# Optimization experiments

Measured on AMD Instinct MI355X. Metric: run time of the kernel, lower is better.

The kernel has to match this reference:

```python
import jax, jax.numpy as jnp
import numpy as np

KERNEL_MUL = 2.0
KERNEL_NUM = 5


def setup_inputs() -> dict:
    key = jax.random.key(0)
    k1, k2 = jax.random.split(key)
    B, Ns, Nt, K = 4, 2048, 2048, 32
    source = jax.random.normal(k1, (B, Ns, K), dtype=jnp.float32)
    target = jax.random.normal(k2, (B, Nt, K), dtype=jnp.float32)
    return {"source": source, "target": target}


def _mmd_rbf(source, target):
    # source: [B, Ns, K], target: [B, Nt, K]
    Ns = source.shape[1]
    Nt = target.shape[1]
    n_samples = Ns + Nt
    total = jnp.concatenate([source, target], axis=1)  # [B, N, K]
    # Pairwise squared L2 via Gram trick (avoids [B, N, N, K] broadcast tensor)
    sq = jnp.sum(total * total, axis=-1)  # [B, N]
    gram = jnp.einsum('bik,bjk->bij', total, total)  # [B, N, N]
    L2 = sq[:, :, None] + sq[:, None, :] - 2.0 * gram  # [B, N, N]
    # Multi-bandwidth RBF kernel sum
    bw = jnp.sum(L2, axis=(1, 2), keepdims=True) / (n_samples ** 2 - n_samples + 1e-8)  # [B,1,1]
    bw = bw / (KERNEL_MUL ** (KERNEL_NUM // 2))
    # Small fixed loop over bandwidths; accumulate to avoid [K_num, B, N, N] stack.
    kernel = jnp.zeros_like(L2)
    for i in range(KERNEL_NUM):
        kernel = kernel + jnp.exp(-L2 / (bw * (KERNEL_MUL ** i)) + 1e-8)
    # Quadrant means
    N = Ns
    XX = kernel[:, :N, :N].mean(axis=(1, 2))
    YY = kernel[:, N:, N:].mean(axis=(1, 2))
    XY = kernel[:, :N, N:].mean(axis=(1, 2))
    YX = kernel[:, N:, :N].mean(axis=(1, 2))
    return XX + YY - XY - YX  # [B]


def reference(source, target):
    return _mmd_rbf(source, target)
```

## Files before the change

### kernel.cpp

```cpp
#include <hip/hip_runtime.h>
#include <hip/hip_bf16.h>


#define NPTS 4096
#define HALF 2048
#define KDIM 32
#define T3   128
#define NTB3 32
#define NPAIR3 528
#define GRIDX 176
#define SPREAD 64

#define WS_SQ    0
#define WS_PART  65536
#define WS_QUAD  133120
#define WS_FRAG  147456
#define WS_NEED  (147456 + 4 * NPTS * 128)

typedef __attribute__((ext_vector_type(8))) short short8v;
typedef __attribute__((ext_vector_type(4))) float f32x4;

__device__ __forceinline__ float fast_exp2(float x) {
#if __has_builtin(__builtin_amdgcn_exp2f)
  return __builtin_amdgcn_exp2f(x);
#else
  return exp2f(x);
#endif
}

__device__ __forceinline__ unsigned int bf16_rne(float x) {
  unsigned int u = __float_as_uint(x);
  return (u + 0x7fffu + ((u >> 16) & 1u)) >> 16;
}

__device__ __forceinline__ const float* point_ptr(const float* __restrict__ src,
                                                  const float* __restrict__ tgt,
                                                  int b, int p) {
  return (p < HALF) ? src + ((size_t)b * HALF + p) * KDIM
                    : tgt + ((size_t)b * HALF + (p - HALF)) * KDIM;
}

__global__ void __launch_bounds__(64)
mmd_pass1(const float* __restrict__ src, const float* __restrict__ tgt,
          float* __restrict__ sqArr, double* __restrict__ part1,
          double* __restrict__ quadbuf,
          unsigned char* __restrict__ frags, int preFlag) {
  const int b = blockIdx.y;
  const int tid = threadIdx.x;
  const int p = blockIdx.x * 64 + tid;

  if (blockIdx.x == 0) {
#pragma unroll
    for (int i = 0; i < 4; ++i)
      quadbuf[b * 4 * SPREAD + i * 64 + tid] = 0.0;
  }

  const float* __restrict__ xp = point_ptr(src, tgt, b, p);
  float x[KDIM];
#pragma unroll
  for (int q = 0; q < 8; ++q) {
    float4 v = reinterpret_cast<const float4*>(xp)[q];
    x[4*q+0] = v.x; x[4*q+1] = v.y; x[4*q+2] = v.z; x[4*q+3] = v.w;
  }
  float s0 = 0.f, s1 = 0.f, s2 = 0.f, s3 = 0.f;
#pragma unroll
  for (int q = 0; q < 8; ++q) {
    s0 = fmaf(x[4*q+0], x[4*q+0], s0);
    s1 = fmaf(x[4*q+1], x[4*q+1], s1);
    s2 = fmaf(x[4*q+2], x[4*q+2], s2);
    s3 = fmaf(x[4*q+3], x[4*q+3], s3);
  }
  const float sq = (s0 + s1) + (s2 + s3);
  sqArr[(size_t)b * NPTS + p] = sq;

  if (preFlag) {
    unsigned int hw[16], lw[16];
#pragma unroll
    for (int e = 0; e < 16; ++e) {
      const float xa = x[2*e], xb = x[2*e+1];
      const unsigned int ha = bf16_rne(xa);
      const unsigned int la = bf16_rne(xa - __uint_as_float(ha << 16));
      const unsigned int hb = bf16_rne(xb);
      const unsigned int lb = bf16_rne(xb - __uint_as_float(hb << 16));
      hw[e] = ha | (hb << 16);
      lw[e] = la | (lb << 16);
    }
    uint4* dst = reinterpret_cast<uint4*>(frags + (size_t)(b * NPTS + p) * 128);
#pragma unroll
    for (int c = 0; c < 4; ++c)
      dst[c] = make_uint4(hw[4*c], hw[4*c+1], hw[4*c+2], hw[4*c+3]);
#pragma unroll
    for (int c = 0; c < 4; ++c)
      dst[4 + c] = make_uint4(lw[4*c], lw[4*c+1], lw[4*c+2], lw[4*c+3]);
  }

  __shared__ float lx[64][KDIM + 1];
#pragma unroll
  for (int k = 0; k < KDIM; ++k) lx[tid][k] = x[k];
  __syncthreads();

  double* slot = part1 + ((size_t)b * 64 + blockIdx.x) * 33;
  if (tid < 32) {
    float ps = 0.f;
#pragma unroll 16
    for (int r = 0; r < 64; ++r) ps += lx[r][tid];
    slot[1 + tid] = (double)ps;
  }
  float w = sq;
#pragma unroll
  for (int off = 32; off > 0; off >>= 1) w += __shfl_down(w, off, 64);
  if (tid == 0) slot[0] = (double)w;
}

__device__ __forceinline__ short8v lds_frag(const unsigned char* base, int p,
                                            int half, int lk) {
  const int slot = (half * 4 + lk) ^ (p & 7);
  return *reinterpret_cast<const short8v*>(base + p * 128 + slot * 16);
}

template <bool PRE>
__global__ void __launch_bounds__(512, 6)
mmd_pass3(const float* __restrict__ src, const float* __restrict__ tgt,
          const float* __restrict__ sqArr, const double* __restrict__ part1,
          const unsigned char* __restrict__ frags,
          double* __restrict__ quadbuf) {
  const int bid = blockIdx.x;
  const int b = blockIdx.y;
  const int tid = threadIdx.x;
  const int lane = tid & 63;
  const int w = tid >> 6;
  const int lm = lane & 15;
  const int lk = lane >> 4;
  const int wr = w & 3;
  const int wc = w >> 2;

  __shared__ __align__(16) unsigned char fragA[T3 * 128];
  __shared__ __align__(16) unsigned char fragB[T3 * 128];
  __shared__ float s_sqA[T3], s_sqB[T3];
  __shared__ double red[33];
  __shared__ float s_nc4;
  __shared__ double wsum[8];

  const float* __restrict__ sqG = sqArr + (size_t)b * NPTS;
  const uint4* __restrict__ gfr =
      reinterpret_cast<const uint4*>(frags) + (size_t)b * NPTS * 8;

  if (tid < 33) {
    double s = 0.0;
#pragma unroll 16
    for (int blk = 0; blk < 64; ++blk)
      s += part1[((size_t)b * 64 + blk) * 33 + tid];
    red[tid] = s;
  }
  __syncthreads();
  if (tid == 0) {
    double ssq = red[0], s2 = 0.0;
    for (int k = 1; k <= 32; ++k) s2 += red[k] * red[k];
    const double N = (double)NPTS;
    double bw = (2.0 * N * ssq - 2.0 * s2) / (N * N - N + 1e-8);
    bw *= 0.25;
    s_nc4 = (float)(-1.4426950408889634 / (bw * 16.0));
  }

  int bxA[3], byA[3];
#pragma unroll
  for (int it = 0; it < 3; ++it) {
    const int pi = bid + it * GRIDX;
    int y = (int)((sqrtf((float)(8 * pi + 1)) - 1.0f) * 0.5f);
    while ((y + 1) * (y + 2) / 2 <= pi) ++y;
    while (y * (y + 1) / 2 > pi) --y;
    byA[it] = y; bxA[it] = pi - y * (y + 1) / 2;
  }

  {
    const int bx = bxA[0], by = byA[0];
    if constexpr (PRE) {
#pragma unroll
      for (int i = 0; i < 2; ++i) {
        const int g = tid + i * 512;
        const int p = g >> 3, s = g & 7;
        const int d = p * 8 + (s ^ (p & 7));
        reinterpret_cast<uint4*>(fragA)[d] = gfr[(size_t)bx * 1024 + g];
        reinterpret_cast<uint4*>(fragB)[d] = gfr[(size_t)by * 1024 + g];
      }
    } else if (tid < 256) {
      const int pt = tid & 127;
      const bool isB = tid >= 128;
      const float* fp = point_ptr(src, tgt, b, (isB ? by : bx) * T3 + pt);
      unsigned int hw[16], lw[16];
#pragma unroll
      for (int e = 0; e < 16; ++e) {
        const float xa = fp[2*e], xb = fp[2*e+1];
        const unsigned int ha = bf16_rne(xa);
        const unsigned int la = bf16_rne(xa - __uint_as_float(ha << 16));
        const unsigned int hb = bf16_rne(xb);
        const unsigned int lb = bf16_rne(xb - __uint_as_float(hb << 16));
        hw[e] = ha | (hb << 16);
        lw[e] = la | (lb << 16);
      }
      uint4* dst = reinterpret_cast<uint4*>((isB ? fragB : fragA) + pt * 128);
#pragma unroll
      for (int s = 0; s < 8; ++s) {
        const unsigned int* s4 = (s < 4) ? &hw[s * 4] : &lw[(s - 4) * 4];
        dst[s ^ (pt & 7)] = make_uint4(s4[0], s4[1], s4[2], s4[3]);
      }
    }
    if (tid < 128) s_sqA[tid] = sqG[bx * T3 + tid];
    else if (tid < 256) s_sqB[tid - 128] = sqG[by * T3 + (tid - 128)];
  }
  __syncthreads();

  const float nc4 = s_nc4;
  const float m2nc = -2.0f * nc4;

  for (int it = 0; it < 3; ++it) {
    const int bx = bxA[it], by = byA[it];

    double accd = 0.0;
#pragma unroll
    for (int cg = 0; cg < 4; ++cg) {
      const int pb = wc * 64 + cg * 16 + lm;
      const short8v Bh = lds_frag(fragB, pb, 0, lk);
      const short8v Bl = lds_frag(fragB, pb, 1, lk);
      const float sjn = s_sqB[pb] * nc4;
#pragma unroll
      for (int rg = 0; rg < 2; ++rg) {
        const int pa = wr * 32 + rg * 16 + lm;
        const short8v Ah = lds_frag(fragA, pa, 0, lk);
        const short8v Al = lds_frag(fragA, pa, 1, lk);
        const float4 sqi4 = *reinterpret_cast<const float4*>(
            &s_sqA[wr * 32 + rg * 16 + lk * 4]);
        const float sin_[4] = {sqi4.x * nc4, sqi4.y * nc4,
                               sqi4.z * nc4, sqi4.w * nc4};
        f32x4 accP = {0.f, 0.f, 0.f, 0.f};
        f32x4 accQ = {0.f, 0.f, 0.f, 0.f};
        accP = __builtin_amdgcn_mfma_f32_16x16x32_bf16(Ah, Bh, accP, 0, 0, 0);
        accQ = __builtin_amdgcn_mfma_f32_16x16x32_bf16(Ah, Bl, accQ, 0, 0, 0);
        accP = __builtin_amdgcn_mfma_f32_16x16x32_bf16(Al, Bl, accP, 0, 0, 0);
        accQ = __builtin_amdgcn_mfma_f32_16x16x32_bf16(Al, Bh, accQ, 0, 0, 0);
        float rs = 0.f;
#pragma unroll
        for (int reg = 0; reg < 4; ++reg) {
          const float dot = accP[reg] + accQ[reg];
          const float arg = fmaf(dot, m2nc, sin_[reg] + sjn);
          float e = fast_exp2(arg);
          float s = e;
          e *= e; s += e;
          e *= e; s += e;
          e *= e; s += e;
          e *= e; s += e;
          rs += s;
        }
        accd += (double)rs;
      }
    }

#pragma unroll
    for (int off = 32; off > 0; off >>= 1) accd += __shfl_down(accd, off, 64);
    if (lane == 0) wsum[w] = accd;

    __syncthreads();

    if (tid == 0) {
      double tot = 0.0;
#pragma unroll
      for (int ww = 0; ww < 8; ++ww) tot += wsum[ww];
      const int rh = (bx >= NTB3 / 2) ? 1 : 0;
      const int ch = (by >= NTB3 / 2) ? 1 : 0;
      const int q  = (rh << 1) | ch;
      const int qT = (ch << 1) | rh;
      const int slot = (bx + by * NTB3) & (SPREAD - 1);
      atomicAdd(&quadbuf[(((b << 2) | q) * SPREAD) + slot], tot);
      if (bx != by)
        atomicAdd(&quadbuf[(((b << 2) | qT) * SPREAD) + slot], tot);
    }

    if (it + 1 < 3) {
      const int nbx = bxA[it + 1], nby = byA[it + 1];
      if constexpr (PRE) {
#pragma unroll
        for (int i = 0; i < 2; ++i) {
          const int g = tid + i * 512;
          const int p = g >> 3, s = g & 7;
          const int d = p * 8 + (s ^ (p & 7));
          reinterpret_cast<uint4*>(fragA)[d] = gfr[(size_t)nbx * 1024 + g];
          reinterpret_cast<uint4*>(fragB)[d] = gfr[(size_t)nby * 1024 + g];
        }
      } else if (tid < 256) {
        const int pt = tid & 127;
        const bool isB = tid >= 128;
        const float* fp = point_ptr(src, tgt, b, (isB ? nby : nbx) * T3 + pt);
        unsigned int hw[16], lw[16];
#pragma unroll
        for (int e = 0; e < 16; ++e) {
          const float xa = fp[2*e], xb = fp[2*e+1];
          const unsigned int ha = bf16_rne(xa);
          const unsigned int la = bf16_rne(xa - __uint_as_float(ha << 16));
          const unsigned int hb = bf16_rne(xb);
          const unsigned int lb = bf16_rne(xb - __uint_as_float(hb << 16));
          hw[e] = ha | (hb << 16);
          lw[e] = la | (lb << 16);
        }
        uint4* dst = reinterpret_cast<uint4*>((isB ? fragB : fragA) + pt * 128);
#pragma unroll
        for (int s = 0; s < 8; ++s) {
          const unsigned int* s4 = (s < 4) ? &hw[s * 4] : &lw[(s - 4) * 4];
          dst[s ^ (pt & 7)] = make_uint4(s4[0], s4[1], s4[2], s4[3]);
        }
      }
      if (tid < 128) s_sqA[tid] = sqG[nbx * T3 + tid];
      else if (tid < 256) s_sqB[tid - 128] = sqG[nby * T3 + (tid - 128)];
      __syncthreads();
    }
  }
}

__global__ void mmd_pass4(const double* __restrict__ quadbuf, float* __restrict__ out) {
  const int tid = threadIdx.x;
  const int qq = tid >> 6, i = tid & 63;
  __shared__ double wsum[4];
  const double inv = 1.0 / ((double)HALF * (double)HALF);
  for (int b = 0; b < 4; ++b) {
    double v = quadbuf[((b << 2) | qq) * SPREAD + i];
    double sv = (qq == 0 || qq == 3) ? v : -v;
#pragma unroll
    for (int off = 32; off > 0; off >>= 1) sv += __shfl_down(sv, off, 64);
    if ((tid & 63) == 0) wsum[qq] = sv;
    __syncthreads();
    if (tid == 0) out[b] = (float)((wsum[0] + wsum[1] + wsum[2] + wsum[3]) * inv);
    __syncthreads();
  }
}

extern "C" void kernel_launch(void* const* d_in, const int* in_sizes, int n_in,
                              void* d_out, int out_size, void* d_ws, size_t ws_size,
                              hipStream_t stream) {
  const float* src = (const float*)d_in[0];
  const float* tgt = (const float*)d_in[1];
  float* out = (float*)d_out;

  char* ws = (char*)d_ws;
  float*         sqArr   = (float*)(ws + WS_SQ);
  double*        part1   = (double*)(ws + WS_PART);
  double*        quadbuf = (double*)(ws + WS_QUAD);
  unsigned char* frags   = (unsigned char*)(ws + WS_FRAG);

  const int pre = (ws_size >= (size_t)WS_NEED) ? 1 : 0;

  mmd_pass1<<<dim3(64, 4), 64, 0, stream>>>(src, tgt, sqArr, part1,
                                            quadbuf, frags, pre);
  if (pre)
    mmd_pass3<true><<<dim3(GRIDX, 4), 512, 0, stream>>>(src, tgt, sqArr, part1,
                                                        frags, quadbuf);
  else
    mmd_pass3<false><<<dim3(GRIDX, 4), 512, 0, stream>>>(src, tgt, sqArr, part1,
                                                         frags, quadbuf);
  mmd_pass4<<<1, 256, 0, stream>>>(quadbuf, out);
}
```

Measured before the change: 83.75 us.

## Assign row-strip tile runs per block with double-buffered B tiles and register-held A

Blocks now walk a run of up to three consecutive column tiles in the same row strip, so the A tile and its squared norms are loaded once and kept in registers for the whole run. The B tile is double-buffered in LDS and the next tile's global loads are issued before the MFMA/exp work, which hides load latency and removes one barrier per iteration. Each wave now does its own atomicAdd instead of reducing through shared memory, dropping a sync at the cost of more atomics. The grid grows to 187 blocks, and some blocks get fewer than three tiles, so work per block is uneven.

After: 83.97 us. Within noise of the previous version (+0.3%).

```diff
diff --git a/kernel.cpp b/kernel.cpp
--- a/kernel.cpp
+++ b/kernel.cpp
@@ -7,8 +7,7 @@
 #define KDIM 32
 #define T3   128
 #define NTB3 32
-#define NPAIR3 528
-#define GRIDX 176
+#define GRIDX 187
 #define SPREAD 64
 
 #define WS_SQ    0
@@ -134,12 +133,20 @@
   const int wr = w & 3;
   const int wc = w >> 2;
 
+  int rem = bid, bx = 0;
+  for (;;) {
+    const int nseg = (32 - bx + 2) / 3;
+    if (rem < nseg) break;
+    rem -= nseg; ++bx;
+  }
+  const int by0 = bx + rem * 3;
+  const int cnt = min(3, 32 - by0);
+
   __shared__ __align__(16) unsigned char fragA[T3 * 128];
-  __shared__ __align__(16) unsigned char fragB[T3 * 128];
-  __shared__ float s_sqA[T3], s_sqB[T3];
+  __shared__ __align__(16) unsigned char fragB[2][T3 * 128];
+  __shared__ float s_sqA[T3], s_sqB[2][T3];
   __shared__ double red[33];
   __shared__ float s_nc4;
-  __shared__ double wsum[8];
 
   const float* __restrict__ sqG = sqArr + (size_t)b * NPTS;
   const uint4* __restrict__ gfr =
@@ -162,87 +169,94 @@
     s_nc4 = (float)(-1.4426950408889634 / (bw * 16.0));
   }
 
-  int bxA[3], byA[3];
-#pragma unroll
-  for (int it = 0; it < 3; ++it) {
-    const int pi = bid + it * GRIDX;
-    int y = (int)((sqrtf((float)(8 * pi + 1)) - 1.0f) * 0.5f);
-    while ((y + 1) * (y + 2) / 2 <= pi) ++y;
-    while (y * (y + 1) / 2 > pi) --y;
-    byA[it] = y; bxA[it] = pi - y * (y + 1) / 2;
-  }
-
-  {
-    const int bx = bxA[0], by = byA[0];
-    if constexpr (PRE) {
-#pragma unroll
-      for (int i = 0; i < 2; ++i) {
-        const int g = tid + i * 512;
-        const int p = g >> 3, s = g & 7;
-        const int d = p * 8 + (s ^ (p & 7));
-        reinterpret_cast<uint4*>(fragA)[d] = gfr[(size_t)bx * 1024 + g];
-        reinterpret_cast<uint4*>(fragB)[d] = gfr[(size_t)by * 1024 + g];
-      }
-    } else if (tid < 256) {
-      const int pt = tid & 127;
-      const bool isB = tid >= 128;
-      const float* fp = point_ptr(src, tgt, b, (isB ? by : bx) * T3 + pt);
-      unsigned int hw[16], lw[16];
-#pragma unroll
-      for (int e = 0; e < 16; ++e) {
-        const float xa = fp[2*e], xb = fp[2*e+1];
-        const unsigned int ha = bf16_rne(xa);
-        const unsigned int la = bf16_rne(xa - __uint_as_float(ha << 16));
-        const unsigned int hb = bf16_rne(xb);
-        const unsigned int lb = bf16_rne(xb - __uint_as_float(hb << 16));
-        hw[e] = ha | (hb << 16);
-        lw[e] = la | (lb << 16);
-      }
-      uint4* dst = reinterpret_cast<uint4*>((isB ? fragB : fragA) + pt * 128);
-#pragma unroll
-      for (int s = 0; s < 8; ++s) {
-        const unsigned int* s4 = (s < 4) ? &hw[s * 4] : &lw[(s - 4) * 4];
-        dst[s ^ (pt & 7)] = make_uint4(s4[0], s4[1], s4[2], s4[3]);
-      }
-    }
-    if (tid < 128) s_sqA[tid] = sqG[bx * T3 + tid];
-    else if (tid < 256) s_sqB[tid - 128] = sqG[by * T3 + (tid - 128)];
-  }
+  if constexpr (PRE) {
+#pragma unroll
+    for (int i = 0; i < 2; ++i) {
+      const int g = tid + i * 512;
+      const int p = g >> 3, s = g & 7;
+      const int d = p * 8 + (s ^ (p & 7));
+      reinterpret_cast<uint4*>(fragA)[d] = gfr[(size_t)bx * 1024 + g];
+      reinterpret_cast<uint4*>(fragB[0])[d] = gfr[(size_t)by0 * 1024 + g];
+    }
+  } else if (tid < 256) {
+    const int pt = tid & 127;
+    const bool isB = tid >= 128;
+    const float* fp = point_ptr(src, tgt, b, (isB ? by0 : bx) * T3 + pt);
+    unsigned int hw[16], lw[16];
+#pragma unroll
+    for (int e = 0; e < 16; ++e) {
+      const float xa = fp[2*e], xb = fp[2*e+1];
+      const unsigned int ha = bf16_rne(xa);
+      const unsigned int la = bf16_rne(xa - __uint_as_float(ha << 16));
+      const unsigned int hb = bf16_rne(xb);
+      const unsigned int lb = bf16_rne(xb - __uint_as_float(hb << 16));
+      hw[e] = ha | (hb << 16);
+      lw[e] = la | (lb << 16);
+    }
+    uint4* dst = reinterpret_cast<uint4*>((isB ? fragB[0] : fragA) + pt * 128);
+#pragma unroll
+    for (int s = 0; s < 8; ++s) {
+      const unsigned int* s4 = (s < 4) ? &hw[s * 4] : &lw[(s - 4) * 4];
+      dst[s ^ (pt & 7)] = make_uint4(s4[0], s4[1], s4[2], s4[3]);
+    }
+  }
+  if (tid < 128) s_sqA[tid] = sqG[bx * T3 + tid];
+  else if (tid < 256) s_sqB[0][tid - 128] = sqG[by0 * T3 + (tid - 128)];
   __syncthreads();
 
   const float nc4 = s_nc4;
   const float m2nc = -2.0f * nc4;
 
-  for (int it = 0; it < 3; ++it) {
-    const int bx = bxA[it], by = byA[it];
+  short8v Ah[2], Al[2];
+  float sin_[2][4];
+#pragma unroll
+  for (int rg = 0; rg < 2; ++rg) {
+    const int pa = wr * 32 + rg * 16 + lm;
+    Ah[rg] = lds_frag(fragA, pa, 0, lk);
+    Al[rg] = lds_frag(fragA, pa, 1, lk);
+    const float4 q4 = *reinterpret_cast<const float4*>(
+        &s_sqA[wr * 32 + rg * 16 + lk * 4]);
+    sin_[rg][0] = q4.x * nc4; sin_[rg][1] = q4.y * nc4;
+    sin_[rg][2] = q4.z * nc4; sin_[rg][3] = q4.w * nc4;
+  }
+
+  const int rh = (bx >= NTB3 / 2) ? 1 : 0;
+
+  for (int it = 0; it < cnt; ++it) {
+    const int c = it & 1;
+    const int by = by0 + it;
+
+    uint4 pv0, pv1;
+    float nsq = 0.f;
+    const bool hn = (it + 1 < cnt);
+    if (hn) {
+      if constexpr (PRE) {
+        pv0 = gfr[(size_t)(by + 1) * 1024 + tid];
+        pv1 = gfr[(size_t)(by + 1) * 1024 + tid + 512];
+      }
+      if (tid < 128) nsq = sqG[(by + 1) * T3 + tid];
+    }
 
     double accd = 0.0;
 #pragma unroll
     for (int cg = 0; cg < 4; ++cg) {
       const int pb = wc * 64 + cg * 16 + lm;
-      const short8v Bh = lds_frag(fragB, pb, 0, lk);
-      const short8v Bl = lds_frag(fragB, pb, 1, lk);
-      const float sjn = s_sqB[pb] * nc4;
+      const short8v Bh = lds_frag(fragB[c], pb, 0, lk);
+      const short8v Bl = lds_frag(fragB[c], pb, 1, lk);
+      const float sjn = s_sqB[c][pb] * nc4;
 #pragma unroll
       for (int rg = 0; rg < 2; ++rg) {
-        const int pa = wr * 32 + rg * 16 + lm;
-        const short8v Ah = lds_frag(fragA, pa, 0, lk);
-        const short8v Al = lds_frag(fragA, pa, 1, lk);
-        const float4 sqi4 = *reinterpret_cast<const float4*>(
-            &s_sqA[wr * 32 + rg * 16 + lk * 4]);
-        const float sin_[4] = {sqi4.x * nc4, sqi4.y * nc4,
-                               sqi4.z * nc4, sqi4.w * nc4};
         f32x4 accP = {0.f, 0.f, 0.f, 0.f};
         f32x4 accQ = {0.f, 0.f, 0.f, 0.f};
-        accP = __builtin_amdgcn_mfma_f32_16x16x32_bf16(Ah, Bh, accP, 0, 0, 0);
-        accQ = __builtin_amdgcn_mfma_f32_16x16x32_bf16(Ah, Bl, accQ, 0, 0, 0);
-        accP = __builtin_amdgcn_mfma_f32_16x16x32_bf16(Al, Bl, accP, 0, 0, 0);
-        accQ = __builtin_amdgcn_mfma_f32_16x16x32_bf16(Al, Bh, accQ, 0, 0, 0);
+        accP = __builtin_amdgcn_mfma_f32_16x16x32_bf16(Ah[rg], Bh, accP, 0, 0, 0);
+        accQ = __builtin_amdgcn_mfma_f32_16x16x32_bf16(Ah[rg], Bl, accQ, 0, 0, 0);
+        accP = __builtin_amdgcn_mfma_f32_16x16x32_bf16(Al[rg], Bl, accP, 0, 0, 0);
+        accQ = __builtin_amdgcn_mfma_f32_16x16x32_bf16(Al[rg], Bh, accQ, 0, 0, 0);
         float rs = 0.f;
 #pragma unroll
         for (int reg = 0; reg < 4; ++reg) {
           const float dot = accP[reg] + accQ[reg];
-          const float arg = fmaf(dot, m2nc, sin_[reg] + sjn);
+          const float arg = fmaf(dot, m2nc, sin_[rg][reg] + sjn);
           float e = fast_exp2(arg);
           float s = e;
           e *= e; s += e;
@@ -257,39 +271,30 @@
 
 #pragma unroll
     for (int off = 32; off > 0; off >>= 1) accd += __shfl_down(accd, off, 64);
-    if (lane == 0) wsum[w] = accd;
-
-    __syncthreads();
-
-    if (tid == 0) {
-      double tot = 0.0;
-#pragma unroll
-      for (int ww = 0; ww < 8; ++ww) tot += wsum[ww];
-      const int rh = (bx >= NTB3 / 2) ? 1 : 0;
+    if (lane == 0) {
       const int ch = (by >= NTB3 / 2) ? 1 : 0;
       const int q  = (rh << 1) | ch;
       const int qT = (ch << 1) | rh;
-      const int slot = (bx + by * NTB3) & (SPREAD - 1);
-      atomicAdd(&quadbuf[(((b << 2) | q) * SPREAD) + slot], tot);
+      const int slot = (bid * 8 + w) & (SPREAD - 1);
+      atomicAdd(&quadbuf[(((b << 2) | q) * SPREAD) + slot], accd);
       if (bx != by)
-        atomicAdd(&quadbuf[(((b << 2) | qT) * SPREAD) + slot], tot);
-    }
-
-    if (it + 1 < 3) {
-      const int nbx = bxA[it + 1], nby = byA[it + 1];
+        atomicAdd(&quadbuf[(((b << 2) | qT) * SPREAD) + slot], accd);
+    }
+
+    if (hn) {
       if constexpr (PRE) {
-#pragma unroll
-        for (int i = 0; i < 2; ++i) {
-          const int g = tid + i * 512;
+        {
+          const int p = tid >> 3, s = tid & 7;
+          reinterpret_cast<uint4*>(fragB[c ^ 1])[p * 8 + (s ^ (p & 7))] = pv0;
+        }
+        {
+          const int g = tid + 512;
           const int p = g >> 3, s = g & 7;
-          const int d = p * 8 + (s ^ (p & 7));
-          reinterpret_cast<uint4*>(fragA)[d] = gfr[(size_t)nbx * 1024 + g];
-          reinterpret_cast<uint4*>(fragB)[d] = gfr[(size_t)nby * 1024 + g];
-        }
-      } else if (tid < 256) {
-        const int pt = tid & 127;
-        const bool isB = tid >= 128;
-        const float* fp = point_ptr(src, tgt, b, (isB ? nby : nbx) * T3 + pt);
+          reinterpret_cast<uint4*>(fragB[c ^ 1])[p * 8 + (s ^ (p & 7))] = pv1;
+        }
+      } else if (tid < 128) {
+        const int pt = tid;
+        const float* fp = point_ptr(src, tgt, b, (by + 1) * T3 + pt);
         unsigned int hw[16], lw[16];
 #pragma unroll
         for (int e = 0; e < 16; ++e) {
@@ -301,15 +306,14 @@
           hw[e] = ha | (hb << 16);
           lw[e] = la | (lb << 16);
         }
-        uint4* dst = reinterpret_cast<uint4*>((isB ? fragB : fragA) + pt * 128);
+        uint4* dst = reinterpret_cast<uint4*>(fragB[c ^ 1] + pt * 128);
 #pragma unroll
         for (int s = 0; s < 8; ++s) {
           const unsigned int* s4 = (s < 4) ? &hw[s * 4] : &lw[(s - 4) * 4];
           dst[s ^ (pt & 7)] = make_uint4(s4[0], s4[1], s4[2], s4[3]);
         }
       }
-      if (tid < 128) s_sqA[tid] = sqG[nbx * T3 + tid];
-      else if (tid < 256) s_sqB[tid - 128] = sqG[nby * T3 + (tid - 128)];
+      if (tid < 128) s_sqB[c ^ 1][tid] = nsq;
       __syncthreads();
     }
   }
```
